# Optimization experiments

Hardware: AMD Instinct MI355X
Metric: run time of the kernel (lower is better)

The kernel has to match this reference:

```python
import jax, jax.numpy as jnp
import numpy as np

B, I, H, E, V, T = 512, 2560, 512, 300, 8000, 16
SOS = 2

def setup_inputs() -> dict:
    key = jax.random.key(0)
    ks = jax.random.split(key, 12)
    s = lambda k, shape: (jax.random.normal(k, shape, jnp.float32) * 0.05)
    emb = s(ks[2], (V, E)).at[0].set(0.0)  # padding_idx=0
    return dict(
        fused_features=jax.random.normal(ks[0], (B, I), jnp.float32),
        target_answers=jax.random.randint(ks[1], (B, T), 0, V),
        max_len=T,
        embedding=emb,
        W_in=s(ks[3], (H, I)), b_in=jnp.zeros((H,), jnp.float32),
        W_cell=s(ks[4], (H, I)), b_cell=jnp.zeros((H,), jnp.float32),
        W_ih0=s(ks[5], (4 * H, E + H)), W_hh0=s(ks[6], (4 * H, H)),
        b_ih0=jnp.zeros((4 * H,), jnp.float32), b_hh0=jnp.zeros((4 * H,), jnp.float32),
        W_ih1=s(ks[7], (4 * H, H)), W_hh1=s(ks[8], (4 * H, H)),
        b_ih1=jnp.zeros((4 * H,), jnp.float32), b_hh1=jnp.zeros((4 * H,), jnp.float32),
        W_out=s(ks[9], (V, H)), b_out=jnp.zeros((V,), jnp.float32),
    )

def _cell(gates, c):
    # PyTorch LSTM gate order: i, f, g, o
    i, f, g, o = jnp.split(gates, 4, axis=-1)
    c_new = jax.nn.sigmoid(f) * c + jax.nn.sigmoid(i) * jnp.tanh(g)
    h_new = jax.nn.sigmoid(o) * jnp.tanh(c_new)
    return h_new, c_new

def reference(fused_features, target_answers, max_len, embedding,
              W_in, b_in, W_cell, b_cell,
              W_ih0, W_hh0, b_ih0, b_hh0,
              W_ih1, W_hh1, b_ih1, b_hh1,
              W_out, b_out):
    context = fused_features @ W_in.T + b_in          # [B,H]
    cell0 = fused_features @ W_cell.T + b_cell        # [B,H]
    # teacher forcing (ratio=1.0, deterministic): inputs = [SOS, y_0..y_{T-2}]
    words = jnp.concatenate(
        [jnp.full((context.shape[0], 1), SOS, target_answers.dtype),
         target_answers[:, :-1]], axis=1)             # [B,T]
    emb = embedding[words]                            # [B,T,E]
    x = jnp.concatenate(
        [emb, jnp.broadcast_to(context[:, None, :], (emb.shape[0], emb.shape[1], context.shape[1]))],
        axis=-1)                                      # [B,T,E+H]
    # precompute input-side gates for layer 0 in one big GEMM
    xg0 = jnp.einsum('bti,gi->tbg', x, W_ih0) + b_ih0 + b_hh0  # [T,B,4H]

    def step(carry, xg):
        h0, c0, h1, c1 = carry
        h0, c0 = _cell(xg + h0 @ W_hh0.T, c0)
        h1, c1 = _cell(h0 @ W_ih1.T + b_ih1 + b_hh1 + h1 @ W_hh1.T, c1)
        return (h0, c0, h1, c1), h1

    init = (context, cell0, context, cell0)
    _, hs = jax.lax.scan(step, init, xg0)             # hs: [T,B,H]
    logits = jnp.einsum('tbh,vh->btv', hs, W_out) + b_out  # [B,T,V]
    return logits
```

## Files before the change

kernel.cpp:

```cpp
#include <hip/hip_runtime.h>
#include <cstdint>

#define B_   512
#define I_   2560
#define H_   512
#define E_   300
#define EW   320
#define V_   8000
#define VPAD 8064
#define T_   16
#define G4H  2048
#define SOS_ 2

typedef _Float16 f16;
typedef _Float16 f16x8 __attribute__((ext_vector_type(8)));
typedef _Float16 f16x4 __attribute__((ext_vector_type(4)));
typedef float    f32x4 __attribute__((ext_vector_type(4)));

__device__ __forceinline__ float sigmoidf_(float x) {
    return 1.0f / (1.0f + __expf(-x));
}

__device__ __forceinline__ void gload16(const void* g, void* l) {
    __builtin_amdgcn_global_load_lds(
        (const __attribute__((address_space(1))) void*)g,
        (__attribute__((address_space(3))) void*)l,
        16, 0, 0);
}

__global__ __launch_bounds__(256)
void gemm_mfma_f16o(const f16* __restrict__ A, int lda,
                    const f16* __restrict__ Bw, int ldb,
                    f16* __restrict__ C, int ldc,
                    int K,
                    const float* __restrict__ bias1)
{
    __shared__ f16 As[128][32];
    __shared__ f16 Bs[128][32];

    const int tid  = threadIdx.x;
    const int w    = tid >> 6;
    const int lane = tid & 63;
    const int bm   = blockIdx.x * 128;
    const int bn   = blockIdx.y * 128;
    const int wr   = w >> 1;
    const int wc   = w & 1;

    const int srow = lane >> 2;
    const int skel = (lane & 3) * 8;

    const f16* Ag0 = A  + (size_t)(bm + w*32 +      srow) * lda + skel;
    const f16* Ag1 = A  + (size_t)(bm + w*32 + 16 + srow) * lda + skel;
    const f16* Bg0 = Bw + (size_t)(bn + w*32 +      srow) * ldb + skel;
    const f16* Bg1 = Bw + (size_t)(bn + w*32 + 16 + srow) * ldb + skel;
    f16* Al0 = &As[w*32     ][0];
    f16* Al1 = &As[w*32 + 16][0];
    f16* Bl0 = &Bs[w*32     ][0];
    f16* Bl1 = &Bs[w*32 + 16][0];

    const int frow = lane & 15;
    const int fk   = (lane >> 4) * 8;

    f32x4 acc[4][4] = {};

    for (int k0 = 0; k0 < K; k0 += 32) {
        gload16(Ag0 + k0, Al0);
        gload16(Ag1 + k0, Al1);
        gload16(Bg0 + k0, Bl0);
        gload16(Bg1 + k0, Bl1);
        __syncthreads();

        f16x8 af[4], bf[4];
        #pragma unroll
        for (int m = 0; m < 4; ++m)
            af[m] = *reinterpret_cast<const f16x8*>(&As[wr*64 + m*16 + frow][fk]);
        #pragma unroll
        for (int n = 0; n < 4; ++n)
            bf[n] = *reinterpret_cast<const f16x8*>(&Bs[wc*64 + n*16 + frow][fk]);

        #pragma unroll
        for (int m = 0; m < 4; ++m)
            #pragma unroll
            for (int n = 0; n < 4; ++n)
                acc[m][n] = __builtin_amdgcn_mfma_f32_16x16x32_f16(
                    af[m], bf[n], acc[m][n], 0, 0, 0);

        __syncthreads();
    }

    const int rowb = bm + wr*64 + (lane >> 4) * 4;
    #pragma unroll
    for (int n = 0; n < 4; ++n) {
        const int col = bn + wc*64 + n*16 + frow;
        const float badd = bias1 ? bias1[col] : 0.0f;
        #pragma unroll
        for (int m = 0; m < 4; ++m) {
            const int r0 = rowb + m*16;
            #pragma unroll
            for (int r = 0; r < 4; ++r)
                C[(size_t)(r0 + r) * ldc + col] = (f16)(acc[m][n][r] + badd);
        }
    }
}

__global__ __launch_bounds__(256)
void gemm_ctx_init(const f16* __restrict__ A,
                   const f16* __restrict__ Bw,
                   const float* __restrict__ b_in,
                   const float* __restrict__ b_cell,
                   f16* __restrict__ ctx16,
                   f16* __restrict__ h0, f16* __restrict__ h1,
                   float* __restrict__ c0, float* __restrict__ c1)
{
    __shared__ f16 As[128][32];
    __shared__ f16 Bs[128][32];

    const int tid  = threadIdx.x;
    const int w    = tid >> 6;
    const int lane = tid & 63;
    const int bm   = blockIdx.x * 128;
    const int bn   = blockIdx.y * 128;
    const int wr   = w >> 1;
    const int wc   = w & 1;

    const int srow = lane >> 2;
    const int skel = (lane & 3) * 8;

    const f16* Ag0 = A  + (size_t)(bm + w*32 +      srow) * I_ + skel;
    const f16* Ag1 = A  + (size_t)(bm + w*32 + 16 + srow) * I_ + skel;
    const f16* Bg0 = Bw + (size_t)(bn + w*32 +      srow) * I_ + skel;
    const f16* Bg1 = Bw + (size_t)(bn + w*32 + 16 + srow) * I_ + skel;
    f16* Al0 = &As[w*32     ][0];
    f16* Al1 = &As[w*32 + 16][0];
    f16* Bl0 = &Bs[w*32     ][0];
    f16* Bl1 = &Bs[w*32 + 16][0];

    const int frow = lane & 15;
    const int fk   = (lane >> 4) * 8;

    f32x4 acc[4][4] = {};

    for (int k0 = 0; k0 < I_; k0 += 32) {
        gload16(Ag0 + k0, Al0);
        gload16(Ag1 + k0, Al1);
        gload16(Bg0 + k0, Bl0);
        gload16(Bg1 + k0, Bl1);
        __syncthreads();

        f16x8 af[4], bf[4];
        #pragma unroll
        for (int m = 0; m < 4; ++m)
            af[m] = *reinterpret_cast<const f16x8*>(&As[wr*64 + m*16 + frow][fk]);
        #pragma unroll
        for (int n = 0; n < 4; ++n)
            bf[n] = *reinterpret_cast<const f16x8*>(&Bs[wc*64 + n*16 + frow][fk]);

        #pragma unroll
        for (int m = 0; m < 4; ++m)
            #pragma unroll
            for (int n = 0; n < 4; ++n)
                acc[m][n] = __builtin_amdgcn_mfma_f32_16x16x32_f16(
                    af[m], bf[n], acc[m][n], 0, 0, 0);

        __syncthreads();
    }

    const int rowb = bm + wr*64 + (lane >> 4) * 4;
    #pragma unroll
    for (int n = 0; n < 4; ++n) {
        const int col = bn + wc*64 + n*16 + frow;
        #pragma unroll
        for (int m = 0; m < 4; ++m) {
            const int r0 = rowb + m*16;
            #pragma unroll
            for (int r = 0; r < 4; ++r) {
                const int row = r0 + r;
                if (col < 512) {
                    const f16 ch = (f16)(acc[m][n][r] + b_in[col]);
                    ctx16[(size_t)row * 512 + col] = ch;
                    h0[(size_t)row * 512 + col] = ch;
                    h1[(size_t)row * 512 + col] = ch;
                } else {
                    const float cc = acc[m][n][r] + b_cell[col - 512];
                    c0[(size_t)row * 512 + col - 512] = cc;
                    c1[(size_t)row * 512 + col - 512] = cc;
                }
            }
        }
    }
}

__device__ __forceinline__ void gemm_cell_body(
    const f16* __restrict__ Ap1, const f16* __restrict__ Ap2, int lda2,
    const f16* __restrict__ Wp, int K,
    const f16* __restrict__ Cadd,
    const float* __restrict__ bih, const float* __restrict__ bhh,
    float* __restrict__ cst,
    f16* __restrict__ hout1,
    char* smem, int bm, int bn)
{
    const int tid  = threadIdx.x;
    const int w    = tid >> 6;
    const int lane = tid & 63;
    const int wr   = w >> 1, wc = w & 1;
    const int frow = lane & 15, hi = lane >> 4;
    const int sw   = (frow & 7) << 4;
    const int srow8 = lane >> 3;
    const int ksb  = ((((lane & 7) * 16) ^ (srow8 << 4)) >> 1);

    const int NT = K >> 6;
    f32x4 acc[2][4] = {};

    char* Abuf = smem;
    char* Wbuf = smem + 24576;

    auto stage = [&](int bsel, int kt) {
        const int k0 = kt << 6;
        #pragma unroll
        for (int j = 0; j < 2; ++j) {
            const int row = w*16 + j*8 + srow8;
            const f16* src;
            if (k0 < 512) src = Ap1 + (size_t)(bm + row) * 512  + k0 + ksb;
            else          src = Ap2 + (size_t)(bm + row) * lda2 + (k0 - 512) + ksb;
            gload16(src, Abuf + bsel*8192 + (w*2 + j)*1024 + lane*16);
        }
        #pragma unroll
        for (int j = 0; j < 4; ++j) {
            const int row = w*32 + j*8 + srow8;
            gload16(Wp + (size_t)(bn + row) * K + k0 + ksb,
                    Wbuf + bsel*16384 + (w*4 + j)*1024 + lane*16);
        }
    };

    stage(0, 0);
    stage(1, 1);
    stage(2, 2);

    int buf = 0;
    for (int kt = 0; kt < NT; ++kt) {
        const int rem = NT - 1 - kt;
        if (rem >= 2)      asm volatile("s_waitcnt vmcnt(12)" ::: "memory");
        else if (rem == 1) asm volatile("s_waitcnt vmcnt(6)" ::: "memory");
        else               asm volatile("s_waitcnt vmcnt(0)" ::: "memory");
        __builtin_amdgcn_sched_barrier(0);
        __builtin_amdgcn_s_barrier();
        __builtin_amdgcn_sched_barrier(0);

        const char* A_ = Abuf + buf*8192;
        const char* W_ = Wbuf + buf*16384;
        f16x8 af[2][2], bf[2][4];
        #pragma unroll
        for (int ks = 0; ks < 2; ++ks) {
            const int cb = (ks*64 + hi*16) ^ sw;
            #pragma unroll
            for (int m = 0; m < 2; ++m)
                af[ks][m] = *reinterpret_cast<const f16x8*>(A_ + (wr*32 + m*16 + frow)*128 + cb);
            #pragma unroll
            for (int n = 0; n < 4; ++n)
                bf[ks][n] = *reinterpret_cast<const f16x8*>(W_ + (wc*64 + n*16 + frow)*128 + cb);
        }
        __builtin_amdgcn_sched_barrier(0);
        asm volatile("s_waitcnt lgkmcnt(0)" ::: "memory");
        __builtin_amdgcn_sched_barrier(0);
        __builtin_amdgcn_s_barrier();
        __builtin_amdgcn_sched_barrier(0);

        if (kt + 3 < NT) stage(buf, kt + 3);

        #pragma unroll
        for (int ks = 0; ks < 2; ++ks)
            #pragma unroll
            for (int m = 0; m < 2; ++m)
                #pragma unroll
                for (int n = 0; n < 4; ++n)
                    acc[m][n] = __builtin_amdgcn_mfma_f32_16x16x32_f16(
                        af[ks][m], bf[ks][n], acc[m][n], 0, 0, 0);
        buf = (buf == 2) ? 0 : buf + 1;
    }

    float* gs = (float*)smem;
    #pragma unroll
    for (int m = 0; m < 2; ++m) {
        const int row = wr*32 + m*16 + hi*4;
        #pragma unroll
        for (int n = 0; n < 4; ++n) {
            const int col = wc*64 + n*16 + frow;
            #pragma unroll
            for (int r = 0; r < 4; ++r) {
                float v = acc[m][n][r];
                if (Cadd) v += (float)Cadd[(size_t)(bm + row + r) * G4H + bn + col];
                gs[(row + r)*132 + col] = v;
            }
        }
    }
    __syncthreads();

    const int hp = tid & 31;
    const int hg = (bn >> 2) + hp;
    float bi0 = 0.f, bi1 = 0.f, bi2 = 0.f, bi3 = 0.f;
    if (bih) {
        bi0 = bih[hg]        + bhh[hg];
        bi1 = bih[512 + hg]  + bhh[512 + hg];
        bi2 = bih[1024 + hg] + bhh[1024 + hg];
        bi3 = bih[1536 + hg] + bhh[1536 + hg];
    }
    #pragma unroll
    for (int i = 0; i < 8; ++i) {
        const int r = (tid >> 5) * 8 + i;
        const int b = bm + r;
        const float gi = gs[r*132 +      hp] + bi0;
        const float gf = gs[r*132 + 32 + hp] + bi1;
        const float gc = gs[r*132 + 64 + hp] + bi2;
        const float go = gs[r*132 + 96 + hp] + bi3;
        const float c  = cst[(size_t)b * 512 + hg];
        const float cn = sigmoidf_(gf) * c + sigmoidf_(gi) * tanhf(gc);
        const float hn = sigmoidf_(go) * tanhf(cn);
        cst[(size_t)b * 512 + hg] = cn;
        hout1[(size_t)b * 512 + hg] = (f16)hn;
    }
}

__device__ __forceinline__ void gemm_out_body(
    const f16* __restrict__ A, const f16* __restrict__ Bw,
    float* __restrict__ C,
    const float* __restrict__ bias,
    int bm, int bn, char* smem, int tid)
{
    const int w    = tid >> 6;
    const int lane = tid & 63;
    const int wr   = w >> 1, wc = w & 1;
    const int frow = lane & 15, hi = lane >> 4;
    const int sw   = (frow & 7) << 4;
    const int srow8 = lane >> 3;
    const int ksb  = ((((lane & 7) * 16) ^ (srow8 << 4)) >> 1);

    char* Abuf = smem;
    char* Wbuf = smem + 32768;
    f32x4 acc[4][4] = {};

    auto stage = [&](int bsel, int kt) {
        const int k0 = kt << 6;
        #pragma unroll
        for (int j = 0; j < 4; ++j) {
            const int row = w*32 + j*8 + srow8;
            gload16(A  + (size_t)(bm + row) * 512 + k0 + ksb,
                    Abuf + bsel*16384 + (w*4 + j)*1024 + lane*16);
            gload16(Bw + (size_t)(bn + row) * 512 + k0 + ksb,
                    Wbuf + bsel*16384 + (w*4 + j)*1024 + lane*16);
        }
    };

    stage(0, 0);
    stage(1, 1);

    int buf = 0;
    for (int kt = 0; kt < 8; ++kt) {
        if (kt < 7) asm volatile("s_waitcnt vmcnt(8)" ::: "memory");
        else        asm volatile("s_waitcnt vmcnt(0)" ::: "memory");
        __builtin_amdgcn_sched_barrier(0);
        __builtin_amdgcn_s_barrier();
        __builtin_amdgcn_sched_barrier(0);

        const char* A_ = Abuf + buf*16384;
        const char* W_ = Wbuf + buf*16384;
        f16x8 af[2][4], bf[2][4];
        #pragma unroll
        for (int ks = 0; ks < 2; ++ks) {
            const int cb = (ks*64 + hi*16) ^ sw;
            #pragma unroll
            for (int m = 0; m < 4; ++m)
                af[ks][m] = *reinterpret_cast<const f16x8*>(A_ + (wr*64 + m*16 + frow)*128 + cb);
            #pragma unroll
            for (int n = 0; n < 4; ++n)
                bf[ks][n] = *reinterpret_cast<const f16x8*>(W_ + (wc*64 + n*16 + frow)*128 + cb);
        }
        __builtin_amdgcn_sched_barrier(0);
        asm volatile("s_waitcnt lgkmcnt(0)" ::: "memory");
        __builtin_amdgcn_sched_barrier(0);
        __builtin_amdgcn_s_barrier();
        __builtin_amdgcn_sched_barrier(0);

        if (kt + 2 < 8) stage(buf, kt + 2);

        #pragma unroll
        for (int ks = 0; ks < 2; ++ks)
            #pragma unroll
            for (int m = 0; m < 4; ++m)
                #pragma unroll
                for (int n = 0; n < 4; ++n)
                    acc[m][n] = __builtin_amdgcn_mfma_f32_16x16x32_f16(
                        af[ks][m], bf[ks][n], acc[m][n], 0, 0, 0);
        buf ^= 1;
    }

    const int rowb = bm + wr*64 + (lane >> 4) * 4;
    #pragma unroll
    for (int n = 0; n < 4; ++n) {
        const int col = bn + wc*64 + n*16 + frow;
        if (col >= V_) continue;
        const float badd = bias[col];
        #pragma unroll
        for (int m = 0; m < 4; ++m) {
            const int r0 = rowb + m*16;
            #pragma unroll
            for (int r = 0; r < 4; ++r)
                __builtin_nontemporal_store(
                    acc[m][n][r] + badd,
                    &C[(size_t)(r0 + r) * (T_ * V_) + col]);
        }
    }
}

__global__ __launch_bounds__(256)
void phase_kernel(const f16* __restrict__ h0in,
                  const f16* __restrict__ embt,
                  f16* __restrict__ h0out,
                  const f16* __restrict__ h1in,
                  f16* __restrict__ h1out,
                  const f16* __restrict__ W0p, const f16* __restrict__ W1p,
                  const f16* __restrict__ WoutP,
                  const f16* __restrict__ ctxg,
                  const float* __restrict__ bih1, const float* __restrict__ bhh1,
                  const float* __restrict__ b_out,
                  float* __restrict__ c0, float* __restrict__ c1,
                  float* __restrict__ out, int tout,
                  int bx0, int active0, int active1, int activeO)
{
    __shared__ char smem[73728];
    const int bx = blockIdx.x + bx0;

    if (bx < 128) {
        if (!active0) return;
        const int xcd = bx & 7, idx = bx >> 3;
        const int bn = (xcd*2 + (idx & 1)) * 128;
        const int bm = (idx >> 1) * 64;
        gemm_cell_body(h0in, embt, EW, W0p, 832,
                       ctxg, nullptr, nullptr, c0, h0out, smem, bm, bn);
    } else if (bx < 256) {
        if (!active1) return;
        const int lb = bx - 128;
        const int xcd = lb & 7, idx = lb >> 3;
        const int bn = (xcd*2 + (idx & 1)) * 128;
        const int bm = (idx >> 1) * 64;
        gemm_cell_body(h0in, h1in, 512, W1p, 1024,
                       nullptr, bih1, bhh1, c1, h1out, smem, bm, bn);
    } else {
        if (!activeO) return;
        const int o = bx - 256;
        const int xcd = o & 7, j = o >> 3;
        const int bnt = xcd*8 + (j >> 2);
        if (bnt >= 63) return;
        const int bm = (j & 3) * 128;
        gemm_out_body(h1in, WoutP, out + (size_t)tout * V_, b_out,
                      bm, bnt * 128, smem, threadIdx.x);
    }
}

#define NB_F16   1280
#define NB_WIC   2560
#define NB_W0    6656
#define NB_W1    8192
#define NB_WCTX  4096
#define NB_B0    8
#define NB_WOUT  4032
#define NB_EMB   10240
#define NB_TOTAL (NB_F16+NB_WIC+NB_W0+NB_W1+NB_WCTX+NB_B0+NB_WOUT+NB_EMB)

__global__ __launch_bounds__(256)
void pack_all(const float* __restrict__ fused,
              const float* __restrict__ Win, const float* __restrict__ Wcell,
              const float* __restrict__ Whh0, const float* __restrict__ Wih0,
              const float* __restrict__ Wih1, const float* __restrict__ Whh1,
              const float* __restrict__ bih0, const float* __restrict__ bhh0,
              const float* __restrict__ Wout,
              const float* __restrict__ emb, const int* __restrict__ target,
              f16* __restrict__ fused16, f16* __restrict__ WinCell,
              f16* __restrict__ W0, f16* __restrict__ W1,
              f16* __restrict__ Wc, float* __restrict__ b01p,
              f16* __restrict__ Wo, f16* __restrict__ embAll)
{
    int bx = blockIdx.x;
    const int tid = threadIdx.x;

    if (bx < NB_F16) {
        const int i = bx * 256 + tid;
        const float4 v = reinterpret_cast<const float4*>(fused)[i];
        f16x4 h = { (f16)v.x, (f16)v.y, (f16)v.z, (f16)v.w };
        *reinterpret_cast<f16x4*>(fused16 + (size_t)i * 4) = h;
        return;
    }
    bx -= NB_F16;
    if (bx < NB_WIC) {
        const int i = bx * 256 + tid;
        const int r = i / 640, c4 = (i % 640) * 4;
        const float* src = (r < 512) ? Win + (size_t)r * I_ + c4
                                     : Wcell + (size_t)(r - 512) * I_ + c4;
        const float4 v = *reinterpret_cast<const float4*>(src);
        f16x4 h = { (f16)v.x, (f16)v.y, (f16)v.z, (f16)v.w };
        *reinterpret_cast<f16x4*>(WinCell + (size_t)i * 4) = h;
        return;
    }
    bx -= NB_WIC;
    if (bx < NB_W0) {
        const int idx = bx * 256 + tid;
        const int rp = idx / 832, k = idx % 832;
        const int g = (rp >> 5) & 3, h = (rp >> 7) * 32 + (rp & 31);
        const int srow = g * 512 + h;
        float v;
        if (k < 512)      v = Whh0[(size_t)srow * 512 + k];
        else if (k < 812) v = Wih0[(size_t)srow * 812 + (k - 512)];
        else              v = 0.0f;
        W0[idx] = (f16)v;
        return;
    }
    bx -= NB_W0;
    if (bx < NB_W1) {
        const int idx = bx * 256 + tid;
        const int rp = idx >> 10, k = idx & 1023;
        const int g = (rp >> 5) & 3, h = (rp >> 7) * 32 + (rp & 31);
        const int srow = g * 512 + h;
        const float v = (k < 512) ? Wih1[(size_t)srow * 512 + k]
                                  : Whh1[(size_t)srow * 512 + (k - 512)];
        W1[idx] = (f16)v;
        return;
    }
    bx -= NB_W1;
    if (bx < NB_WCTX) {
        const int idx = bx * 256 + tid;
        const int rp = idx >> 9, k = idx & 511;
        const int g = (rp >> 5) & 3, h = (rp >> 7) * 32 + (rp & 31);
        Wc[idx] = (f16)Wih0[(size_t)(g * 512 + h) * 812 + 300 + k];
        return;
    }
    bx -= NB_WCTX;
    if (bx < NB_B0) {
        const int idx = bx * 256 + tid;
        const int g = (idx >> 5) & 3, h = (idx >> 7) * 32 + (idx & 31);
        b01p[idx] = bih0[g * 512 + h] + bhh0[g * 512 + h];
        return;
    }
    bx -= NB_B0;
    if (bx < NB_WOUT) {
        const int i = bx * 256 + tid;
        const int r = i >> 7, c4 = (i & 127) * 4;
        f16x4 h = { (f16)0.f, (f16)0.f, (f16)0.f, (f16)0.f };
        if (r < V_) {
            const float4 v = *reinterpret_cast<const float4*>(Wout + (size_t)r * H_ + c4);
            h = f16x4{ (f16)v.x, (f16)v.y, (f16)v.z, (f16)v.w };
        }
        *reinterpret_cast<f16x4*>(Wo + (size_t)i * 4) = h;
        return;
    }
    bx -= NB_WOUT;
    {
        const int idx = bx * 256 + tid;
        const int t = idx / (B_ * EW);
        const int rem = idx % (B_ * EW);
        const int b = rem / EW, e = rem % EW;
        const int wd = (t == 0) ? SOS_ : target[b * T_ + (t - 1)];
        const float v = (e < E_) ? emb[(size_t)wd * E_ + e] : 0.0f;
        embAll[idx] = (f16)v;
    }
}

extern "C" void kernel_launch(void* const* d_in, const int* in_sizes, int n_in,
                              void* d_out, int out_size, void* d_ws, size_t ws_size,
                              hipStream_t stream)
{
    const float* fused  = (const float*)d_in[0];
    const int*   target = (const int*)d_in[1];
    const float* emb    = (const float*)d_in[3];
    const float* W_in   = (const float*)d_in[4];
    const float* b_in   = (const float*)d_in[5];
    const float* W_cell = (const float*)d_in[6];
    const float* b_cell = (const float*)d_in[7];
    const float* W_ih0  = (const float*)d_in[8];
    const float* W_hh0  = (const float*)d_in[9];
    const float* b_ih0  = (const float*)d_in[10];
    const float* b_hh0  = (const float*)d_in[11];
    const float* W_ih1  = (const float*)d_in[12];
    const float* W_hh1  = (const float*)d_in[13];
    const float* b_ih1  = (const float*)d_in[14];
    const float* b_hh1  = (const float*)d_in[15];
    const float* W_out  = (const float*)d_in[16];
    const float* b_out  = (const float*)d_in[17];
    float* out = (float*)d_out;

    char* p = (char*)d_ws;
    auto carve = [&](size_t bytes) {
        char* r = p;
        p += (bytes + 255) & ~(size_t)255;
        return r;
    };
    f16* ctxg     = (f16*)carve((size_t)B_ * G4H * 2);
    float* b01p   = (float*)carve((size_t)G4H * 4);
    float* c0     = (float*)carve((size_t)B_ * H_ * 4);
    float* c1     = (float*)carve((size_t)B_ * H_ * 4);
    f16* fused16  = (f16*)carve((size_t)B_ * I_ * 2);
    f16* WinCell  = (f16*)carve((size_t)1024 * I_ * 2);
    f16* W0p      = (f16*)carve((size_t)G4H * 832 * 2);
    f16* W1p      = (f16*)carve((size_t)G4H * 1024 * 2);
    f16* Wctxp    = (f16*)carve((size_t)G4H * H_ * 2);
    f16* Wout16   = (f16*)carve((size_t)VPAD * H_ * 2);
    f16* ctx16    = (f16*)carve((size_t)B_ * H_ * 2);
    f16* h0a      = (f16*)carve((size_t)B_ * H_ * 2);
    f16* h0b      = (f16*)carve((size_t)B_ * H_ * 2);
    f16* h1a      = (f16*)carve((size_t)B_ * H_ * 2);
    f16* h1b      = (f16*)carve((size_t)B_ * H_ * 2);
    f16* embAll   = (f16*)carve((size_t)T_ * B_ * EW * 2);

    pack_all<<<dim3(NB_TOTAL), 256, 0, stream>>>(
        fused, W_in, W_cell, W_hh0, W_ih0, W_ih1, W_hh1,
        b_ih0, b_hh0, W_out, emb, target,
        fused16, WinCell, W0p, W1p, Wctxp, b01p, Wout16, embAll);

    gemm_ctx_init<<<dim3(B_/128, 1024/128), 256, 0, stream>>>(
        fused16, WinCell, b_in, b_cell, ctx16, h0b, h1b, c0, c1);

    gemm_mfma_f16o<<<dim3(B_/128, G4H/128), 256, 0, stream>>>(
        ctx16, H_, Wctxp, H_, ctxg, G4H, H_, b01p);

    f16* h0buf[2] = { h0a, h0b };
    f16* h1buf[2] = { h1a, h1b };
    for (int phase = 0; phase <= T_ + 1; ++phase) {
        const int a0 = (phase < T_) ? 1 : 0;
        const int a1 = (phase >= 1 && phase <= T_) ? 1 : 0;
        const int aO = (phase >= 2) ? 1 : 0;
        const int te = (phase < T_) ? phase : (T_ - 1);
        const int tO = aO ? (phase - 2) : 0;
        int bx0 = 0, nb = 512;
        if (phase == 0)            { bx0 = 0;   nb = 128; }
        else if (phase == 1)       { bx0 = 0;   nb = 256; }
        else if (phase == T_)      { bx0 = 128; nb = 384; }
        else if (phase == T_ + 1)  { bx0 = 256; nb = 256; }
        phase_kernel<<<dim3(nb), 256, 0, stream>>>(
            h0buf[(phase + 1) & 1],
            embAll + (size_t)te * B_ * EW,
            h0buf[phase & 1],
            h1buf[phase & 1],
            h1buf[(phase + 1) & 1],
            W0p, W1p, Wout16, ctxg, b_ih1, b_hh1, b_out,
            c0, c1, out, tO, bx0, a0, a1, aO);
    }
}
```

Before: 417.6 us.

## Single-barrier GEMM pipeline with prefetch depth two and vectorized weight packing

The GEMM main loop moves from three stages in flight with two barriers per k-step to two stages in flight with one barrier. It stages into the buffer consumed on the previous iteration, so the second barrier and the lgkmcnt wait are no longer needed, and a __syncthreads is added before the epilogue reuses shared memory. Separately, the pack kernel's scalar weight and embedding conversion loops become float4-to-f16x4 vector loads and stores, which cuts the block counts by four. The shallower prefetch may expose more global-load latency, and the vector loads on Wih0 rows with a 300 offset depend on alignment.

```diff
diff --git a/kernel.cpp b/kernel.cpp
--- a/kernel.cpp
+++ b/kernel.cpp
@@ -234,20 +234,17 @@
 
     stage(0, 0);
     stage(1, 1);
-    stage(2, 2);
-
-    int buf = 0;
+
+    int rb = 0;
     for (int kt = 0; kt < NT; ++kt) {
-        const int rem = NT - 1 - kt;
-        if (rem >= 2)      asm volatile("s_waitcnt vmcnt(12)" ::: "memory");
-        else if (rem == 1) asm volatile("s_waitcnt vmcnt(6)" ::: "memory");
-        else               asm volatile("s_waitcnt vmcnt(0)" ::: "memory");
+        if (kt < NT - 1) asm volatile("s_waitcnt vmcnt(6)" ::: "memory");
+        else             asm volatile("s_waitcnt vmcnt(0)" ::: "memory");
         __builtin_amdgcn_sched_barrier(0);
         __builtin_amdgcn_s_barrier();
         __builtin_amdgcn_sched_barrier(0);
 
-        const char* A_ = Abuf + buf*8192;
-        const char* W_ = Wbuf + buf*16384;
+        const char* A_ = Abuf + rb*8192;
+        const char* W_ = Wbuf + rb*16384;
         f16x8 af[2][2], bf[2][4];
         #pragma unroll
         for (int ks = 0; ks < 2; ++ks) {
@@ -259,13 +256,11 @@
             for (int n = 0; n < 4; ++n)
                 bf[ks][n] = *reinterpret_cast<const f16x8*>(W_ + (wc*64 + n*16 + frow)*128 + cb);
         }
-        __builtin_amdgcn_sched_barrier(0);
-        asm volatile("s_waitcnt lgkmcnt(0)" ::: "memory");
-        __builtin_amdgcn_sched_barrier(0);
-        __builtin_amdgcn_s_barrier();
-        __builtin_amdgcn_sched_barrier(0);
-
-        if (kt + 3 < NT) stage(buf, kt + 3);
+
+        if (kt + 2 < NT) {
+            int sb = rb - 1; if (sb < 0) sb = 2;
+            stage(sb, kt + 2);
+        }
 
         #pragma unroll
         for (int ks = 0; ks < 2; ++ks)
@@ -275,8 +270,9 @@
                 for (int n = 0; n < 4; ++n)
                     acc[m][n] = __builtin_amdgcn_mfma_f32_16x16x32_f16(
                         af[ks][m], bf[ks][n], acc[m][n], 0, 0, 0);
-        buf = (buf == 2) ? 0 : buf + 1;
-    }
+        rb = (rb == 2) ? 0 : rb + 1;
+    }
+    __syncthreads();
 
     float* gs = (float*)smem;
     #pragma unroll
@@ -458,12 +454,12 @@
 
 #define NB_F16   1280
 #define NB_WIC   2560
-#define NB_W0    6656
-#define NB_W1    8192
-#define NB_WCTX  4096
+#define NB_W0    1664
+#define NB_W1    2048
+#define NB_WCTX  1024
 #define NB_B0    8
 #define NB_WOUT  4032
-#define NB_EMB   10240
+#define NB_EMB   2560
 #define NB_TOTAL (NB_F16+NB_WIC+NB_W0+NB_W1+NB_WCTX+NB_B0+NB_WOUT+NB_EMB)
 
 __global__ __launch_bounds__(256)
@@ -482,11 +478,14 @@
     int bx = blockIdx.x;
     const int tid = threadIdx.x;
 
+    auto cvt4 = [](float4 v) {
+        return f16x4{ (f16)v.x, (f16)v.y, (f16)v.z, (f16)v.w };
+    };
+
     if (bx < NB_F16) {
         const int i = bx * 256 + tid;
-        const float4 v = reinterpret_cast<const float4*>(fused)[i];
-        f16x4 h = { (f16)v.x, (f16)v.y, (f16)v.z, (f16)v.w };
-        *reinterpret_cast<f16x4*>(fused16 + (size_t)i * 4) = h;
+        *reinterpret_cast<f16x4*>(fused16 + (size_t)i * 4) =
+            cvt4(reinterpret_cast<const float4*>(fused)[i]);
         return;
     }
     bx -= NB_F16;
@@ -495,41 +494,44 @@
         const int r = i / 640, c4 = (i % 640) * 4;
         const float* src = (r < 512) ? Win + (size_t)r * I_ + c4
                                      : Wcell + (size_t)(r - 512) * I_ + c4;
-        const float4 v = *reinterpret_cast<const float4*>(src);
-        f16x4 h = { (f16)v.x, (f16)v.y, (f16)v.z, (f16)v.w };
-        *reinterpret_cast<f16x4*>(WinCell + (size_t)i * 4) = h;
+        *reinterpret_cast<f16x4*>(WinCell + (size_t)i * 4) =
+            cvt4(*reinterpret_cast<const float4*>(src));
         return;
     }
     bx -= NB_WIC;
     if (bx < NB_W0) {
         const int idx = bx * 256 + tid;
-        const int rp = idx / 832, k = idx % 832;
+        const int rp = idx / 208, k = (idx % 208) * 4;
         const int g = (rp >> 5) & 3, h = (rp >> 7) * 32 + (rp & 31);
         const int srow = g * 512 + h;
-        float v;
-        if (k < 512)      v = Whh0[(size_t)srow * 512 + k];
-        else if (k < 812) v = Wih0[(size_t)srow * 812 + (k - 512)];
-        else              v = 0.0f;
-        W0[idx] = (f16)v;
+        f16x4 o = { (f16)0.f, (f16)0.f, (f16)0.f, (f16)0.f };
+        if (k < 512)
+            o = cvt4(*reinterpret_cast<const float4*>(Whh0 + (size_t)srow * 512 + k));
+        else if (k < 812)
+            o = cvt4(*reinterpret_cast<const float4*>(Wih0 + (size_t)srow * 812 + (k - 512)));
+        *reinterpret_cast<f16x4*>(W0 + (size_t)rp * 832 + k) = o;
         return;
     }
     bx -= NB_W0;
     if (bx < NB_W1) {
         const int idx = bx * 256 + tid;
-        const int rp = idx >> 10, k = idx & 1023;
+        const int rp = idx >> 8, k = (idx & 255) * 4;
         const int g = (rp >> 5) & 3, h = (rp >> 7) * 32 + (rp & 31);
         const int srow = g * 512 + h;
-        const float v = (k < 512) ? Wih1[(size_t)srow * 512 + k]
-                                  : Whh1[(size_t)srow * 512 + (k - 512)];
-        W1[idx] = (f16)v;
+        const float* src = (k < 512) ? Wih1 + (size_t)srow * 512 + k
+                                     : Whh1 + (size_t)srow * 512 + (k - 512);
+        *reinterpret_cast<f16x4*>(W1 + (size_t)rp * 1024 + k) =
+            cvt4(*reinterpret_cast<const float4*>(src));
         return;
     }
     bx -= NB_W1;
     if (bx < NB_WCTX) {
         const int idx = bx * 256 + tid;
-        const int rp = idx >> 9, k = idx & 511;
+        const int rp = idx >> 7, k = (idx & 127) * 4;
         const int g = (rp >> 5) & 3, h = (rp >> 7) * 32 + (rp & 31);
-        Wc[idx] = (f16)Wih0[(size_t)(g * 512 + h) * 812 + 300 + k];
+        *reinterpret_cast<f16x4*>(Wc + (size_t)rp * 512 + k) =
+            cvt4(*reinterpret_cast<const float4*>(
+                Wih0 + (size_t)(g * 512 + h) * 812 + 300 + k));
         return;
     }
     bx -= NB_WCTX;
@@ -543,23 +545,23 @@
     if (bx < NB_WOUT) {
         const int i = bx * 256 + tid;
         const int r = i >> 7, c4 = (i & 127) * 4;
-        f16x4 h = { (f16)0.f, (f16)0.f, (f16)0.f, (f16)0.f };
-        if (r < V_) {
-            const float4 v = *reinterpret_cast<const float4*>(Wout + (size_t)r * H_ + c4);
-            h = f16x4{ (f16)v.x, (f16)v.y, (f16)v.z, (f16)v.w };
-        }
-        *reinterpret_cast<f16x4*>(Wo + (size_t)i * 4) = h;
+        f16x4 o = { (f16)0.f, (f16)0.f, (f16)0.f, (f16)0.f };
+        if (r < V_)
+            o = cvt4(*reinterpret_cast<const float4*>(Wout + (size_t)r * H_ + c4));
+        *reinterpret_cast<f16x4*>(Wo + (size_t)i * 4) = o;
         return;
     }
     bx -= NB_WOUT;
     {
         const int idx = bx * 256 + tid;
-        const int t = idx / (B_ * EW);
-        const int rem = idx % (B_ * EW);
-        const int b = rem / EW, e = rem % EW;
+        const int t = idx / (B_ * 80);
+        const int rem = idx % (B_ * 80);
+        const int b = rem / 80, e = (rem % 80) * 4;
         const int wd = (t == 0) ? SOS_ : target[b * T_ + (t - 1)];
-        const float v = (e < E_) ? emb[(size_t)wd * E_ + e] : 0.0f;
-        embAll[idx] = (f16)v;
+        f16x4 o = { (f16)0.f, (f16)0.f, (f16)0.f, (f16)0.f };
+        if (e < E_)
+            o = cvt4(*reinterpret_cast<const float4*>(emb + (size_t)wd * E_ + e));
+        *reinterpret_cast<f16x4*>(embAll + ((size_t)t * B_ + b) * EW + e) = o;
     }
 }
 
```

Measured after the change: 410.0 us, median of 2. About the same (-1.8%).
